# Optimization experiments

Measured on AMD Instinct MI355X. Metric: run time of the kernel, lower is better.

Reference implementation:

```python
import jax, jax.numpy as jnp
from jax import lax
import numpy as np

IN_CH, OUT_CH, K, STRIDE = 4, 256, 16, 8
D_STATE, D_CONV, EXPAND, HEADDIM = 128, 4, 2, 64
D_INNER = EXPAND * OUT_CH            # 512
NHEADS = D_INNER // HEADDIM          # 8
CONV_DIM = D_INNER + 2 * D_STATE     # 768 (ngroups=1)
D_IN_PROJ = 2 * D_INNER + 2 * D_STATE + NHEADS  # 1288
B_SZ, L = 8, 16384


def _conv1d(x, w, b, stride, padding):
    y = lax.conv_general_dilated(x, w, (stride,), padding,
                                 dimension_numbers=('NCH', 'OIH', 'NCH'))
    return y + b[None, :, None]


def _mamba2(u, in_proj_w, conv1d_w, conv1d_b, dt_bias, A_log, D_skip, norm_w, out_proj_w):
    # u: (b, l, d_model). Faithful Mamba2 forward (ngroups=1, rmsnorm gated, no biases on projections).
    b, l, _ = u.shape
    zxbcdt = jnp.einsum('bld,ed->ble', u, in_proj_w)           # (b, l, d_in_proj)
    z = zxbcdt[..., :D_INNER]
    xBC = zxbcdt[..., D_INNER:D_INNER + CONV_DIM]
    dt = jax.nn.softplus(zxbcdt[..., D_INNER + CONV_DIM:] + dt_bias)  # (b, l, h)
    # causal depthwise conv (torch pads d_conv-1 both sides then truncates to :l == left-pad only) + SiLU
    xBC = lax.conv_general_dilated(xBC.transpose(0, 2, 1), conv1d_w, (1,),
                                   [(D_CONV - 1, 0)], feature_group_count=CONV_DIM,
                                   dimension_numbers=('NCH', 'OIH', 'NCH'))
    xBC = jax.nn.silu((xBC + conv1d_b[None, :, None]).transpose(0, 2, 1))  # (b, l, conv_dim)
    xs = xBC[..., :D_INNER].reshape(b, l, NHEADS, HEADDIM)
    Bm = xBC[..., D_INNER:D_INNER + D_STATE]                   # (b, l, n)
    Cm = xBC[..., D_INNER + D_STATE:]                          # (b, l, n)
    A = -jnp.exp(A_log)                                        # (h,), scalar A per head
    dA = jnp.exp(dt * A)                                       # (b, l, h)

    def step(h, inp):
        dA_t, dt_t, x_t, B_t, C_t = inp
        h = h * dA_t[:, :, None, None] + jnp.einsum('bh,bhp,bn->bhpn', dt_t, x_t, B_t)
        return h, jnp.einsum('bhpn,bn->bhp', h, C_t)

    h0 = jnp.zeros((b, NHEADS, HEADDIM, D_STATE), dtype=u.dtype)
    _, ys = lax.scan(step, h0, (dA.swapaxes(0, 1), dt.swapaxes(0, 1),
                                xs.swapaxes(0, 1), Bm.swapaxes(0, 1), Cm.swapaxes(0, 1)))
    y = ys.swapaxes(0, 1) + D_skip[None, None, :, None] * xs   # (b, l, h, p)
    y = y.reshape(b, l, D_INNER) * jax.nn.silu(z)              # gated RMSNorm (norm_before_gate=False)
    y = y * lax.rsqrt(jnp.mean(y * y, axis=-1, keepdims=True) + 1e-5) * norm_w
    return jnp.einsum('ble,de->bld', y, out_proj_w)


def _forward(x, conv_w, conv_b, in_proj_w, conv1d_w, conv1d_b, dt_bias, A_log,
             D_skip, norm_w, out_proj_w, conv1_w, conv1_b, convT_w, convT_b):
    h = jax.nn.relu(_conv1d(x, conv_w, conv_b, STRIDE, 'VALID'))       # (b, out_ch, l')
    y = _mamba2(h.transpose(0, 2, 1), in_proj_w, conv1d_w, conv1d_b,
                dt_bias, A_log, D_skip, norm_w, out_proj_w)
    y = y.transpose(0, 2, 1)                                           # (b, out_ch, l')
    y = _conv1d(y, conv1_w, conv1_b, 1, [(7, 8)])  # torch padding='same', even kernel: left=7, right=8
    # ConvTranspose1d: torch weight (Cin, Cout, K) -> flipped OIH kernel + lhs dilation
    kern = jnp.flip(convT_w, -1).transpose(1, 0, 2)
    y = lax.conv_general_dilated(y, kern, (1,), [(K - 1, K - 1)], lhs_dilation=(STRIDE,),
                                 dimension_numbers=('NCH', 'OIH', 'NCH'))
    return y + convT_b[None, :, None]


def setup_inputs() -> dict:
    key = jax.random.key(0)
    ks = jax.random.split(key, 16)
    n = lambda k, shp, sc=0.05: jax.random.normal(k, shp, dtype=jnp.float32) * sc
    return {
        'x': jax.random.normal(ks[0], (B_SZ, IN_CH, L), dtype=jnp.float32),
        'conv_w': n(ks[1], (OUT_CH, IN_CH, K)),
        'conv_b': n(ks[2], (OUT_CH,)),
        'in_proj_w': n(ks[3], (D_IN_PROJ, OUT_CH)),
        'conv1d_w': n(ks[4], (CONV_DIM, 1, D_CONV), 0.3),
        'conv1d_b': n(ks[5], (CONV_DIM,), 0.1),
        'dt_bias': n(ks[6], (NHEADS,), 0.5),
        'A_log': jnp.log(jax.random.uniform(ks[7], (NHEADS,), minval=1.0, maxval=16.0)),
        'D_skip': n(ks[8], (NHEADS,), 1.0),
        'norm_w': jnp.ones((D_INNER,), dtype=jnp.float32),
        'out_proj_w': n(ks[9], (OUT_CH, D_INNER)),
        'conv1_w': n(ks[10], (STRIDE, OUT_CH, K)),
        'conv1_b': n(ks[11], (STRIDE,)),
        'convT_w': n(ks[12], (STRIDE, IN_CH, K)),
        'convT_b': n(ks[13], (IN_CH,)),
    }


def reference(x, conv_w, conv_b, in_proj_w, conv1d_w, conv1d_b, dt_bias, A_log,
              D_skip, norm_w, out_proj_w, conv1_w, conv1_b, convT_w, convT_b):
    return _forward(x, conv_w, conv_b, in_proj_w, conv1d_w, conv1d_b, dt_bias, A_log,
                    D_skip, norm_w, out_proj_w, conv1_w, conv1_b, convT_w, convT_b)
```

## Files before the change

### kernel.cpp

```cpp
#include <hip/hip_runtime.h>
#include <cstddef>
#include <cstdint>

constexpr int L_IN   = 16384;
constexpr int L_SEQ  = 2047;
constexpr int BATCH  = 8;
constexpr int M_TOK  = BATCH * L_SEQ;
constexpr int D_INNER = 512;
constexpr int NHEADS  = 8;
constexpr int HEADDIM = 64;
constexpr int D_STATE = 128;
constexpr int CONV_DIM = 768;
constexpr int D_IN_PROJ = 1288;

constexpr int QC  = 64;
constexpr int NCH = 32;

constexpr size_t OFF_U    = 0;
constexpr size_t OFF_PB   = OFF_U   + 2096128;
constexpr size_t OFF_ZB   = OFF_U   + 4192256;
constexpr size_t OFF_XBC  = OFF_ZB  + 4192256;
constexpr size_t OFF_DT   = OFF_XBC + 6288384;
constexpr size_t OFF_AW   = OFF_DT  + 131008;
constexpr size_t OFF_XC   = OFF_AW  + 131008;
constexpr size_t OFF_Y    = OFF_XC  + 6288384;
constexpr size_t OFF_YC1  = OFF_Y   + 4192256;
constexpr size_t OFF_PBUF = OFF_YC1 + 131008;
constexpr size_t OFF_HS   = OFF_PBUF + 2048;
constexpr size_t OFF_WBIN = OFF_HS  + 8388608;
constexpr size_t OFF_WBF  = OFF_WBIN + 164864;
constexpr size_t OFF_W2   = OFF_WBF + 8192;

using short8 = __attribute__((ext_vector_type(8))) short;
using f32x4  = __attribute__((ext_vector_type(4))) float;
typedef unsigned short ushort_t;

__device__ __forceinline__ ushort_t f2bf(float f) {
  uint32_t u = __float_as_uint(f);
  u += 0x7fffu + ((u >> 16) & 1u);
  return (ushort_t)(u >> 16);
}
__device__ __forceinline__ float bf2f(ushort_t h) {
  return __uint_as_float(((uint32_t)h) << 16);
}
#define MFMA16(a, b, c) __builtin_amdgcn_mfma_f32_16x16x32_bf16(a, b, c, 0, 0, 0)

#define GLD_LDS(gp, lp) __builtin_amdgcn_global_load_lds( \
    (const __attribute__((address_space(1))) void*)(gp),  \
    (__attribute__((address_space(3))) void*)(lp), 16, 0, 0)

__global__ __launch_bounds__(256) void k_prep(const float* __restrict__ x,
    const float* __restrict__ w1, const float* __restrict__ w3,
    const float* __restrict__ conv1_w, const float* __restrict__ wout,
    ushort_t* __restrict__ PB, ushort_t* __restrict__ o1, ushort_t* __restrict__ o3,
    ushort_t* __restrict__ W2b) {
  const int bid = blockIdx.x;
  const int tid = threadIdx.x;
  if (bid < 512) {
    int idx = bid * 256 + tid;
    if (idx >= M_TOK * 8) return;
    int oct = idx & 7, row = idx >> 3;
    int t = row % L_SEQ, b = row / L_SEQ;
    int ic = oct >> 1, k0 = (oct & 1) * 8;
    const float* src = x + ((size_t)b * 4 + ic) * L_IN + t * 8 + k0;
    float4 a0 = *(const float4*)src;
    float4 a1 = *(const float4*)(src + 4);
    short8 o;
    o[0] = (short)f2bf(a0.x); o[1] = (short)f2bf(a0.y);
    o[2] = (short)f2bf(a0.z); o[3] = (short)f2bf(a0.w);
    o[4] = (short)f2bf(a1.x); o[5] = (short)f2bf(a1.y);
    o[6] = (short)f2bf(a1.z); o[7] = (short)f2bf(a1.w);
    *(short8*)(PB + (size_t)row * 64 + oct * 8) = o;
  } else if (bid < 1800) {
    int i = (bid - 512) * 256 + tid;
    if (i < D_IN_PROJ * 256) o1[i] = f2bf(w1[i]);
    if (i < 256 * 64)        o3[i] = f2bf(w3[i]);
  } else {
    const int r = bid - 1800;
    const int oc = r >> 4, k = r & 15;
    const int d0 = tid;
    float acc0 = 0.f, acc1 = 0.f;
    for (int o = 0; o < 256; o++) {
      float wv = conv1_w[((size_t)oc * 256 + o) * 16 + k];
      acc0 = fmaf(wv, wout[(size_t)o * 512 + d0], acc0);
      acc1 = fmaf(wv, wout[(size_t)o * 512 + d0 + 256], acc1);
    }
    W2b[(size_t)r * 512 + d0]       = f2bf(acc0);
    W2b[(size_t)r * 512 + d0 + 256] = f2bf(acc1);
  }
}

template<int EPI>
__global__ __launch_bounds__(256) void gemm_bf16(const ushort_t* __restrict__ A, int lda,
    const ushort_t* __restrict__ B, int ldb, float* __restrict__ C,
    const float* __restrict__ bias, int M, int N, int K, int nx,
    ushort_t* __restrict__ zb, ushort_t* __restrict__ xbcb,
    float* __restrict__ dtb, float* __restrict__ awb,
    const float* __restrict__ dt_bias, const float* __restrict__ A_log) {
  __shared__ __attribute__((aligned(16))) ushort_t sA[128 * 64];
  __shared__ __attribute__((aligned(16))) ushort_t sB[128 * 64];
  const int tid = threadIdx.x;
  const int cpx = gridDim.x >> 3;
  const int swz = (blockIdx.x & 7) * cpx + (blockIdx.x >> 3);
  const int m0 = (swz / nx) * 128, n0 = (swz % nx) * 128;
  const int w = tid >> 6, lane = tid & 63;
  const int l15 = lane & 15, lK = lane >> 4;
  const int wr = w >> 1, wc = w & 1;
  f32x4 acc[4][4] = {};
  for (int k0 = 0; k0 < K; k0 += 64) {
    __syncthreads();
#pragma unroll
    for (int j = 0; j < 4; j++) {
      int idx = j * 256 + tid;
      int r = idx >> 3;
      int ss = (idx & 7) ^ (r & 7);
      GLD_LDS(A + (size_t)(m0 + r) * lda + k0 + ss * 8, &sA[(j * 256 + w * 64) * 8]);
      GLD_LDS(B + (size_t)(n0 + r) * ldb + k0 + ss * 8, &sB[(j * 256 + w * 64) * 8]);
    }
    __syncthreads();
#pragma unroll
    for (int kk = 0; kk < 2; kk++) {
      short8 af[4], bf[4];
#pragma unroll
      for (int mt = 0; mt < 4; mt++) {
        int r = wr * 64 + mt * 16 + l15;
        af[mt] = *(const short8*)&sA[r * 64 + (((kk * 4 + lK) ^ (r & 7)) * 8)];
      }
#pragma unroll
      for (int nt = 0; nt < 4; nt++) {
        int r = wc * 64 + nt * 16 + l15;
        bf[nt] = *(const short8*)&sB[r * 64 + (((kk * 4 + lK) ^ (r & 7)) * 8)];
      }
#pragma unroll
      for (int mt = 0; mt < 4; mt++)
#pragma unroll
        for (int nt = 0; nt < 4; nt++)
          acc[mt][nt] = MFMA16(af[mt], bf[nt], acc[mt][nt]);
    }
  }
  if constexpr (EPI == 0) {
#pragma unroll
    for (int mt = 0; mt < 4; mt++)
#pragma unroll
      for (int i = 0; i < 4; i++) {
        int gm = m0 + wr * 64 + mt * 16 + lK * 4 + i;
        if (gm < M) {
          float* crow = C + (size_t)gm * N;
#pragma unroll
          for (int nt = 0; nt < 4; nt++) {
            int gn = n0 + wc * 64 + nt * 16 + l15;
            if (gn < N) crow[gn] = acc[mt][nt][i];
          }
        }
      }
  } else if constexpr (EPI == 1) {
    ushort_t* Cb = (ushort_t*)C;
#pragma unroll
    for (int mt = 0; mt < 4; mt++)
#pragma unroll
      for (int i = 0; i < 4; i++) {
        int gm = m0 + wr * 64 + mt * 16 + lK * 4 + i;
#pragma unroll
        for (int nt = 0; nt < 4; nt++) {
          int gn = n0 + wc * 64 + nt * 16 + l15;
          float v = fmaxf(acc[mt][nt][i] + bias[gn], 0.f);
          uint32_t mine = f2bf(v);
          uint32_t other = (uint32_t)__shfl_xor((int)mine, 1, 64);
          if (((lane & 1) == 0) && gm < M)
            *(uint32_t*)(Cb + (size_t)gm * N + gn) = mine | (other << 16);
        }
      }
  } else {
    if (n0 < 1280) {
      ushort_t* dst = (n0 < 512) ? zb : xbcb;
      const int ldd  = (n0 < 512) ? 512 : 768;
      const int coff = (n0 < 512) ? 0 : 512;
#pragma unroll
      for (int mt = 0; mt < 4; mt++)
#pragma unroll
        for (int i = 0; i < 4; i++) {
          int gm = m0 + wr * 64 + mt * 16 + lK * 4 + i;
#pragma unroll
          for (int nt = 0; nt < 4; nt++) {
            int gn = n0 + wc * 64 + nt * 16 + l15;
            uint32_t mine = f2bf(acc[mt][nt][i]);
            uint32_t other = (uint32_t)__shfl_xor((int)mine, 1, 64);
            if (((lane & 1) == 0) && gm < M)
              *(uint32_t*)(dst + (size_t)gm * ldd + (gn - coff)) = mine | (other << 16);
          }
        }
    } else {
#pragma unroll
      for (int mt = 0; mt < 4; mt++)
#pragma unroll
        for (int i = 0; i < 4; i++) {
          int gm = m0 + wr * 64 + mt * 16 + lK * 4 + i;
          if (gm >= M) continue;
#pragma unroll
          for (int nt = 0; nt < 4; nt++) {
            int gn = n0 + wc * 64 + nt * 16 + l15;
            if (gn < N) {
              int hd = gn - 1280;
              float v = acc[mt][nt][i] + dt_bias[hd];
              float sp = (v > 20.f) ? v : log1pf(expf(v));
              dtb[(size_t)gm * 8 + hd] = sp;
              awb[(size_t)gm * 8 + hd] = -expf(A_log[hd]) * sp;
            }
          }
        }
    }
  }
}

__global__ __launch_bounds__(192) void k_dw(const ushort_t* __restrict__ xbcb,
    const float* __restrict__ w, const float* __restrict__ bias,
    ushort_t* __restrict__ xcb) {
  const int bid = blockIdx.x;
  const int tb = bid & 511, b = bid >> 9;
  const int t0 = tb * 4;
  const int c = threadIdx.x * 4;
  const size_t rowb = (size_t)b * L_SEQ;
  float wr[4][4];
#pragma unroll
  for (int j = 0; j < 4; j++)
#pragma unroll
    for (int k = 0; k < 4; k++) wr[j][k] = w[(c + j) * 4 + k];
  const float4 bs = {bias[c], bias[c + 1], bias[c + 2], bias[c + 3]};
  float v[7][4];
#pragma unroll
  for (int r = 0; r < 7; r++) {
    int tt = t0 - 3 + r;
    if (tt >= 0 && tt < L_SEQ) {
      uint2 pk = *(const uint2*)(xbcb + (rowb + tt) * CONV_DIM + c);
      v[r][0] = bf2f((ushort_t)(pk.x & 0xffff));
      v[r][1] = bf2f((ushort_t)(pk.x >> 16));
      v[r][2] = bf2f((ushort_t)(pk.y & 0xffff));
      v[r][3] = bf2f((ushort_t)(pk.y >> 16));
    } else {
      v[r][0] = v[r][1] = v[r][2] = v[r][3] = 0.f;
    }
  }
#pragma unroll
  for (int o = 0; o < 4; o++) {
    int t = t0 + o;
    if (t >= L_SEQ) break;
    float a0 = bs.x, a1 = bs.y, a2 = bs.z, a3 = bs.w;
#pragma unroll
    for (int k = 0; k < 4; k++) {
      a0 = fmaf(v[o + k][0], wr[0][k], a0);
      a1 = fmaf(v[o + k][1], wr[1][k], a1);
      a2 = fmaf(v[o + k][2], wr[2][k], a2);
      a3 = fmaf(v[o + k][3], wr[3][k], a3);
    }
    float s0 = a0 / (1.f + expf(-a0));
    float s1 = a1 / (1.f + expf(-a1));
    float s2 = a2 / (1.f + expf(-a2));
    float s3 = a3 / (1.f + expf(-a3));
    uint2 ov;
    ov.x = (uint32_t)f2bf(s0) | ((uint32_t)f2bf(s1) << 16);
    ov.y = (uint32_t)f2bf(s2) | ((uint32_t)f2bf(s3) << 16);
    *(uint2*)(xcb + (rowb + t) * CONV_DIM + c) = ov;
  }
}

__global__ __launch_bounds__(256) void k_ssd_state(const ushort_t* __restrict__ xcb,
    const float* __restrict__ dtb, const float* __restrict__ aw,
    ushort_t* __restrict__ HSb, float* __restrict__ Pbuf) {
  const int ch = blockIdx.x, bh = blockIdx.y;
  const int b = bh >> 3, h = bh & 7;
  const int t0 = ch * QC;
  const int valid = (L_SEQ - t0 < QC) ? (L_SEQ - t0) : QC;
  const size_t rowbase = (size_t)b * L_SEQ;
  __shared__ __attribute__((aligned(16))) short sBT[128][72];
  __shared__ __attribute__((aligned(16))) short sXw[64][72];
  __shared__ float sW[64];
  __shared__ float sLtot;
  const int tid = threadIdx.x;
  if (tid < 64) {
    float aa = 0.f, dd = 0.f;
    if (tid < valid) { size_t r8 = (rowbase + t0 + tid) * 8 + h; aa = aw[r8]; dd = dtb[r8]; }
    float s = aa;
#pragma unroll
    for (int d = 1; d < 64; d <<= 1) { float o = __shfl_up(s, d, 64); if (tid >= d) s += o; }
    float Lt = __shfl(s, 63, 64);
    sW[tid] = expf(Lt - s) * dd;
    if (tid == 63) sLtot = s;
  }
  __syncthreads();
  for (int i = tid; i < 64 * 16; i += 256) {
    int r = i >> 4, q = (i & 15) * 8;
    short8 v = {0, 0, 0, 0, 0, 0, 0, 0};
    if (r < valid) v = *(const short8*)(xcb + (rowbase + t0 + r) * CONV_DIM + 512 + q);
#pragma unroll
    for (int j = 0; j < 8; j++) sBT[q + j][r] = v[j];
  }
  for (int i = tid; i < 64 * 8; i += 256) {
    int r = i >> 3, q = (i & 7) * 8;
    short8 v = {0, 0, 0, 0, 0, 0, 0, 0};
    if (r < valid) v = *(const short8*)(xcb + (rowbase + t0 + r) * CONV_DIM + h * 64 + q);
    float wv = sW[r];
#pragma unroll
    for (int j = 0; j < 8; j++) sXw[q + j][r] = (short)f2bf(bf2f((ushort_t)v[j]) * wv);
  }
  __syncthreads();
  const int w = tid >> 6, l15 = tid & 15, lK = (tid & 63) >> 4;
  f32x4 acc[2][4] = {};
  short8 afr[2][2];
#pragma unroll
  for (int j = 0; j < 2; j++)
#pragma unroll
    for (int kt = 0; kt < 2; kt++)
      afr[j][kt] = *(const short8*)&sBT[(w * 2 + j) * 16 + l15][kt * 32 + lK * 8];
#pragma unroll
  for (int pt = 0; pt < 4; pt++) {
#pragma unroll
    for (int kt = 0; kt < 2; kt++) {
      short8 bfr = *(const short8*)&sXw[pt * 16 + l15][kt * 32 + lK * 8];
      acc[0][pt] = MFMA16(afr[0][kt], bfr, acc[0][pt]);
      acc[1][pt] = MFMA16(afr[1][kt], bfr, acc[1][pt]);
    }
  }
  ushort_t* dst = HSb + ((size_t)bh * NCH + ch) * 8192;
#pragma unroll
  for (int j = 0; j < 2; j++)
#pragma unroll
    for (int pt = 0; pt < 4; pt++)
#pragma unroll
      for (int i = 0; i < 4; i++) {
        int n = (w * 2 + j) * 16 + lK * 4 + i, p = pt * 16 + l15;
        uint32_t mine = f2bf(acc[j][pt][i]);
        uint32_t other = (uint32_t)__shfl_xor((int)mine, 1, 64);
        if ((l15 & 1) == 0)
          *(uint32_t*)(dst + n * 64 + p) = mine | (other << 16);
      }
  if (tid == 0) Pbuf[bh * NCH + ch] = expf(sLtot);
}

__global__ __launch_bounds__(256) void k_ssd_comb(ushort_t* __restrict__ HSb,
                                                  const float* __restrict__ Pbuf) {
  const int bh = blockIdx.y;
  const int e2 = blockIdx.x * 256 + threadIdx.x;
  const size_t base = (size_t)bh * NCH * 8192 + (size_t)e2 * 2;
  uint32_t pk[NCH];
  float P[NCH];
#pragma unroll
  for (int c = 0; c < NCH; c++) pk[c] = *(const uint32_t*)(HSb + base + (size_t)c * 8192);
#pragma unroll
  for (int c = 0; c < NCH; c++) P[c] = Pbuf[bh * NCH + c];
  float run0 = 0.f, run1 = 0.f;
#pragma unroll
  for (int c = 0; c < NCH; c++) {
    run0 = fmaf(P[c], run0, bf2f((ushort_t)(pk[c] & 0xffff)));
    run1 = fmaf(P[c], run1, bf2f((ushort_t)(pk[c] >> 16)));
    pk[c] = (uint32_t)f2bf(run0) | ((uint32_t)f2bf(run1) << 16);
  }
#pragma unroll
  for (int c = 0; c < NCH; c++) *(uint32_t*)(HSb + base + (size_t)c * 8192) = pk[c];
}

__global__ __launch_bounds__(256) void k_ssd_y(const ushort_t* __restrict__ xcb,
    const float* __restrict__ dtb, const float* __restrict__ aw,
    const float* __restrict__ Dskip, const ushort_t* __restrict__ HSb,
    ushort_t* __restrict__ y16) {
  const int ch = blockIdx.x, bh = blockIdx.y;
  const int b = bh >> 3, h = bh & 7;
  const int t0 = ch * QC;
  const int valid = (L_SEQ - t0 < QC) ? (L_SEQ - t0) : QC;
  const size_t rowbase = (size_t)b * L_SEQ;
  __shared__ __attribute__((aligned(16))) short sB[64][136];
  __shared__ __attribute__((aligned(16))) short sC[64][136];
  __shared__ __attribute__((aligned(16))) short sH[64][136];
  __shared__ __attribute__((aligned(16))) short sX[64][72];
  __shared__ float sLrel[64], sdt[64], sEL[64];
  short (*sM)[72] = (short(*)[72])&sB[0][0];
  const int tid = threadIdx.x;
  if (tid < 64) {
    float aa = 0.f, dd = 0.f;
    if (tid < valid) { size_t r8 = (rowbase + t0 + tid) * 8 + h; aa = aw[r8]; dd = dtb[r8]; }
    float s = aa;
#pragma unroll
    for (int d = 1; d < 64; d <<= 1) { float o = __shfl_up(s, d, 64); if (tid >= d) s += o; }
    sLrel[tid] = s; sdt[tid] = dd; sEL[tid] = expf(s);
  }
  for (int i = tid; i < 64 * 16; i += 256) {
    int r = i >> 4, q = (i & 15) * 8;
    short8 vb = {0, 0, 0, 0, 0, 0, 0, 0}, vc = {0, 0, 0, 0, 0, 0, 0, 0};
    if (r < valid) {
      const ushort_t* rp = xcb + (rowbase + t0 + r) * CONV_DIM;
      vb = *(const short8*)(rp + 512 + q);
      vc = *(const short8*)(rp + 640 + q);
    }
#pragma unroll
    for (int j = 0; j < 8; j++) { sB[r][q + j] = vb[j]; sC[r][q + j] = vc[j]; }
  }
  for (int i = tid; i < 64 * 8; i += 256) {
    int r = i >> 3, q = (i & 7) * 8;
    short8 v = {0, 0, 0, 0, 0, 0, 0, 0};
    if (r < valid) v = *(const short8*)(xcb + (rowbase + t0 + r) * CONV_DIM + h * 64 + q);
#pragma unroll
    for (int j = 0; j < 8; j++) sX[q + j][r] = v[j];
  }
  for (int i = tid; i < 128 * 8; i += 256) {
    int n = i >> 3, q = (i & 7) * 8;
    short8 v = {0, 0, 0, 0, 0, 0, 0, 0};
    if (ch > 0) v = *(const short8*)(HSb + ((size_t)bh * NCH + (ch - 1)) * 8192 + n * 64 + q);
#pragma unroll
    for (int j = 0; j < 8; j++) sH[q + j][n] = v[j];
  }
  __syncthreads();
  const int w = tid >> 6, l15 = tid & 15, lK = (tid & 63) >> 4;
  short8 aC[4];
#pragma unroll
  for (int kt = 0; kt < 4; kt++)
    aC[kt] = *(const short8*)&sC[w * 16 + l15][kt * 32 + lK * 8];
  f32x4 g[4] = {};
#pragma unroll
  for (int st = 0; st < 4; st++)
#pragma unroll
    for (int kt = 0; kt < 4; kt++)
      g[st] = MFMA16(aC[kt], *(const short8*)&sB[st * 16 + l15][kt * 32 + lK * 8], g[st]);
  __syncthreads();
#pragma unroll
  for (int st = 0; st < 4; st++)
#pragma unroll
    for (int i = 0; i < 4; i++) {
      int tt = w * 16 + lK * 4 + i, ss = st * 16 + l15;
      float f = (ss <= tt) ? expf(sLrel[tt] - sLrel[ss]) * sdt[ss] : 0.f;
      sM[tt][ss] = (short)f2bf(g[st][i] * f);
    }
  __syncthreads();
  f32x4 acc[4] = {};
#pragma unroll
  for (int pt = 0; pt < 4; pt++)
#pragma unroll
    for (int kt = 0; kt < 4; kt++)
      acc[pt] = MFMA16(aC[kt], *(const short8*)&sH[pt * 16 + l15][kt * 32 + lK * 8], acc[pt]);
#pragma unroll
  for (int pt = 0; pt < 4; pt++)
#pragma unroll
    for (int i = 0; i < 4; i++)
      acc[pt][i] *= sEL[w * 16 + lK * 4 + i];
  short8 aM[2];
#pragma unroll
  for (int kt = 0; kt < 2; kt++)
    aM[kt] = *(const short8*)&sM[w * 16 + l15][kt * 32 + lK * 8];
#pragma unroll
  for (int pt = 0; pt < 4; pt++)
#pragma unroll
    for (int kt = 0; kt < 2; kt++)
      acc[pt] = MFMA16(aM[kt], *(const short8*)&sX[pt * 16 + l15][kt * 32 + lK * 8], acc[pt]);
  const float Dsk = Dskip[h];
#pragma unroll
  for (int pt = 0; pt < 4; pt++)
#pragma unroll
    for (int i = 0; i < 4; i++) {
      int tt = w * 16 + lK * 4 + i;
      int pp = pt * 16 + l15;
      float v = acc[pt][i] + Dsk * bf2f((ushort_t)sX[pp][tt]);
      uint32_t mine = f2bf(v);
      uint32_t other = (uint32_t)__shfl_xor((int)mine, 1, 64);
      if (((l15 & 1) == 0) && tt < valid)
        *(uint32_t*)(y16 + (rowbase + t0 + tt) * D_INNER + h * 64 + pp) = mine | (other << 16);
    }
}

__global__ __launch_bounds__(256) void k_norm(ushort_t* __restrict__ y16,
    const ushort_t* __restrict__ zb, const float* __restrict__ norm_w) {
  const int row = blockIdx.x * 4 + (threadIdx.x >> 6);
  const int lane = threadIdx.x & 63;
  const int c0 = lane * 8;
  ushort_t* yrow = y16 + (size_t)row * D_INNER;
  short8 yv = *(const short8*)(yrow + c0);
  short8 zv = *(const short8*)(zb + (size_t)row * 512 + c0);
  float v[8];
  float ss = 0.f;
#pragma unroll
  for (int j = 0; j < 8; j++) {
    float z = bf2f((ushort_t)zv[j]);
    float g = z / (1.f + expf(-z));
    v[j] = bf2f((ushort_t)yv[j]) * g;
    ss += v[j] * v[j];
  }
#pragma unroll
  for (int m = 32; m >= 1; m >>= 1) ss += __shfl_xor(ss, m, 64);
  float scale = rsqrtf(ss * (1.f / 512.f) + 1e-5f);
  float4 nw0 = *(const float4*)(norm_w + c0);
  float4 nw1 = *(const float4*)(norm_w + c0 + 4);
  short8 o;
  o[0] = (short)f2bf(v[0] * scale * nw0.x); o[1] = (short)f2bf(v[1] * scale * nw0.y);
  o[2] = (short)f2bf(v[2] * scale * nw0.z); o[3] = (short)f2bf(v[3] * scale * nw0.w);
  o[4] = (short)f2bf(v[4] * scale * nw1.x); o[5] = (short)f2bf(v[5] * scale * nw1.y);
  o[6] = (short)f2bf(v[6] * scale * nw1.z); o[7] = (short)f2bf(v[7] * scale * nw1.w);
  *(short8*)(yrow + c0) = o;
}

__global__ void k_red(const float* __restrict__ Y, const float* __restrict__ b1,
                      float* __restrict__ yc1) {
  int idx = blockIdx.x * 256 + threadIdx.x;
  if (idx >= BATCH * 8 * L_SEQ) return;
  int t = idx % L_SEQ;
  int bj = idx / L_SEQ;
  int j = bj & 7, b = bj >> 3;
  float acc = b1[j];
  const float* Yb = Y + (size_t)b * L_SEQ * 128;
#pragma unroll
  for (int k = 0; k < 16; k++) {
    int tt = t - 7 + k;
    if (tt >= 0 && tt < L_SEQ) acc += Yb[(size_t)tt * 128 + j * 16 + k];
  }
  yc1[idx] = acc;
}

__global__ void k_convT(const float* __restrict__ yc1,
                        const float* __restrict__ wT,
                        const float* __restrict__ bT, float* __restrict__ out) {
  const int s = blockIdx.x * 256 + threadIdx.x;
  const int c = blockIdx.y, b = blockIdx.z;
  float acc = bT[c];
  const int k0 = (15 - (s & 7)) & 7;
#pragma unroll
  for (int dk = 0; dk < 2; dk++) {
    int k = k0 + 8 * dk;
    int num = s - 15 + k;
    int m = num >> 3;
    if (num >= 0 && m < L_SEQ) {
#pragma unroll
      for (int j = 0; j < 8; j++) {
        float v = yc1[((size_t)b * 8 + j) * L_SEQ + m];
        acc = fmaf(v, wT[((size_t)j * 4 + c) * 16 + (15 - k)], acc);
      }
    }
  }
  out[((size_t)b * 4 + c) * L_IN + s] = acc;
}

extern "C" void kernel_launch(void* const* d_in, const int* in_sizes, int n_in,
                              void* d_out, int out_size, void* d_ws, size_t ws_size,
                              hipStream_t stream) {
  const float* x         = (const float*)d_in[0];
  const float* conv_w    = (const float*)d_in[1];
  const float* conv_b    = (const float*)d_in[2];
  const float* in_proj_w = (const float*)d_in[3];
  const float* conv1d_w  = (const float*)d_in[4];
  const float* conv1d_b  = (const float*)d_in[5];
  const float* dt_bias   = (const float*)d_in[6];
  const float* A_log     = (const float*)d_in[7];
  const float* D_skip    = (const float*)d_in[8];
  const float* norm_w    = (const float*)d_in[9];
  const float* out_proj_w= (const float*)d_in[10];
  const float* conv1_w   = (const float*)d_in[11];
  const float* conv1_b   = (const float*)d_in[12];
  const float* convT_w   = (const float*)d_in[13];
  const float* convT_b   = (const float*)d_in[14];
  float* out = (float*)d_out;
  float* ws  = (float*)d_ws;

  ushort_t* ub   = (ushort_t*)(ws + OFF_U);
  ushort_t* PB   = (ushort_t*)(ws + OFF_PB);
  ushort_t* zb   = (ushort_t*)(ws + OFF_ZB);
  ushort_t* xbcb = (ushort_t*)(ws + OFF_XBC);
  float* dtb  = ws + OFF_DT;
  float* awb  = ws + OFF_AW;
  ushort_t* xcb = (ushort_t*)(ws + OFF_XC);
  ushort_t* y16 = (ushort_t*)(ws + OFF_Y);
  float* yc1  = ws + OFF_YC1;
  float* Pbuf = ws + OFF_PBUF;
  ushort_t* HSb = (ushort_t*)(ws + OFF_HS);
  ushort_t* wbin  = (ushort_t*)(ws + OFF_WBIN);
  ushort_t* wbf   = (ushort_t*)(ws + OFF_WBF);
  ushort_t* W2b   = (ushort_t*)(ws + OFF_W2);
  float* Yg   = ws + OFF_U;

  k_prep<<<dim3(1928), 256, 0, stream>>>(x, in_proj_w, conv_w, conv1_w, out_proj_w,
                                         PB, wbin, wbf, W2b);
  gemm_bf16<1><<<dim3(256), 256, 0, stream>>>(PB, 64, wbf, 64, (float*)ub,
      conv_b, M_TOK, 256, 64, 2, nullptr, nullptr, nullptr, nullptr, nullptr, nullptr);
  gemm_bf16<2><<<dim3(1408), 256, 0, stream>>>(ub, 256, wbin, 256, nullptr,
      nullptr, M_TOK, D_IN_PROJ, 256, 11, zb, xbcb, dtb, awb, dt_bias, A_log);
  k_dw<<<dim3(BATCH * 512), 192, 0, stream>>>(xbcb, conv1d_w, conv1d_b, xcb);
  k_ssd_state<<<dim3(NCH, 64), 256, 0, stream>>>(xcb, dtb, awb, HSb, Pbuf);
  k_ssd_comb<<<dim3(16, 64), 256, 0, stream>>>(HSb, Pbuf);
  k_ssd_y<<<dim3(NCH, 64), 256, 0, stream>>>(xcb, dtb, awb, D_skip, HSb, y16);
  k_norm<<<dim3(M_TOK / 4), 256, 0, stream>>>(y16, zb, norm_w);
  gemm_bf16<0><<<dim3(128), 256, 0, stream>>>(y16, 512, W2b, 512, Yg,
      nullptr, M_TOK, 128, D_INNER, 1, nullptr, nullptr, nullptr, nullptr, nullptr, nullptr);
  k_red<<<dim3((BATCH * 8 * L_SEQ + 255) / 256), 256, 0, stream>>>(Yg, conv1_b, yc1);
  k_convT<<<dim3(64, 4, 8), 256, 0, stream>>>(yc1, convT_w, convT_b, out);
}
```

Baseline: 199.2 us.

## Fuse depthwise conv into SSD kernels, norm into out GEMM, tail reduction into convT

```diff
diff --git a/kernel.cpp b/kernel.cpp
--- a/kernel.cpp
+++ b/kernel.cpp
@@ -43,6 +43,7 @@
 __device__ __forceinline__ float bf2f(ushort_t h) {
   return __uint_as_float(((uint32_t)h) << 16);
 }
+__device__ __forceinline__ float siluf(float a) { return a / (1.f + expf(-a)); }
 #define MFMA16(a, b, c) __builtin_amdgcn_mfma_f32_16x16x32_bf16(a, b, c, 0, 0, 0)
 
 #define GLD_LDS(gp, lp) __builtin_amdgcn_global_load_lds( \
@@ -52,6 +53,7 @@
 __global__ __launch_bounds__(256) void k_prep(const float* __restrict__ x,
     const float* __restrict__ w1, const float* __restrict__ w3,
     const float* __restrict__ conv1_w, const float* __restrict__ wout,
+    const float* __restrict__ norm_w,
     ushort_t* __restrict__ PB, ushort_t* __restrict__ o1, ushort_t* __restrict__ o3,
     ushort_t* __restrict__ W2b) {
   const int bid = blockIdx.x;
@@ -85,8 +87,8 @@
       acc0 = fmaf(wv, wout[(size_t)o * 512 + d0], acc0);
       acc1 = fmaf(wv, wout[(size_t)o * 512 + d0 + 256], acc1);
     }
-    W2b[(size_t)r * 512 + d0]       = f2bf(acc0);
-    W2b[(size_t)r * 512 + d0 + 256] = f2bf(acc1);
+    W2b[(size_t)r * 512 + d0]       = f2bf(acc0 * norm_w[d0]);
+    W2b[(size_t)r * 512 + d0 + 256] = f2bf(acc1 * norm_w[d0 + 256]);
   }
 }
 
@@ -138,22 +140,7 @@
           acc[mt][nt] = MFMA16(af[mt], bf[nt], acc[mt][nt]);
     }
   }
-  if constexpr (EPI == 0) {
-#pragma unroll
-    for (int mt = 0; mt < 4; mt++)
-#pragma unroll
-      for (int i = 0; i < 4; i++) {
-        int gm = m0 + wr * 64 + mt * 16 + lK * 4 + i;
-        if (gm < M) {
-          float* crow = C + (size_t)gm * N;
-#pragma unroll
-          for (int nt = 0; nt < 4; nt++) {
-            int gn = n0 + wc * 64 + nt * 16 + l15;
-            if (gn < N) crow[gn] = acc[mt][nt][i];
-          }
-        }
-      }
-  } else if constexpr (EPI == 1) {
+  if constexpr (EPI == 1) {
     ushort_t* Cb = (ushort_t*)C;
 #pragma unroll
     for (int mt = 0; mt < 4; mt++)
@@ -212,58 +199,8 @@
   }
 }
 
-__global__ __launch_bounds__(192) void k_dw(const ushort_t* __restrict__ xbcb,
-    const float* __restrict__ w, const float* __restrict__ bias,
-    ushort_t* __restrict__ xcb) {
-  const int bid = blockIdx.x;
-  const int tb = bid & 511, b = bid >> 9;
-  const int t0 = tb * 4;
-  const int c = threadIdx.x * 4;
-  const size_t rowb = (size_t)b * L_SEQ;
-  float wr[4][4];
-#pragma unroll
-  for (int j = 0; j < 4; j++)
-#pragma unroll
-    for (int k = 0; k < 4; k++) wr[j][k] = w[(c + j) * 4 + k];
-  const float4 bs = {bias[c], bias[c + 1], bias[c + 2], bias[c + 3]};
-  float v[7][4];
-#pragma unroll
-  for (int r = 0; r < 7; r++) {
-    int tt = t0 - 3 + r;
-    if (tt >= 0 && tt < L_SEQ) {
-      uint2 pk = *(const uint2*)(xbcb + (rowb + tt) * CONV_DIM + c);
-      v[r][0] = bf2f((ushort_t)(pk.x & 0xffff));
-      v[r][1] = bf2f((ushort_t)(pk.x >> 16));
-      v[r][2] = bf2f((ushort_t)(pk.y & 0xffff));
-      v[r][3] = bf2f((ushort_t)(pk.y >> 16));
-    } else {
-      v[r][0] = v[r][1] = v[r][2] = v[r][3] = 0.f;
-    }
-  }
-#pragma unroll
-  for (int o = 0; o < 4; o++) {
-    int t = t0 + o;
-    if (t >= L_SEQ) break;
-    float a0 = bs.x, a1 = bs.y, a2 = bs.z, a3 = bs.w;
-#pragma unroll
-    for (int k = 0; k < 4; k++) {
-      a0 = fmaf(v[o + k][0], wr[0][k], a0);
-      a1 = fmaf(v[o + k][1], wr[1][k], a1);
-      a2 = fmaf(v[o + k][2], wr[2][k], a2);
-      a3 = fmaf(v[o + k][3], wr[3][k], a3);
-    }
-    float s0 = a0 / (1.f + expf(-a0));
-    float s1 = a1 / (1.f + expf(-a1));
-    float s2 = a2 / (1.f + expf(-a2));
-    float s3 = a3 / (1.f + expf(-a3));
-    uint2 ov;
-    ov.x = (uint32_t)f2bf(s0) | ((uint32_t)f2bf(s1) << 16);
-    ov.y = (uint32_t)f2bf(s2) | ((uint32_t)f2bf(s3) << 16);
-    *(uint2*)(xcb + (rowb + t) * CONV_DIM + c) = ov;
-  }
-}
-
-__global__ __launch_bounds__(256) void k_ssd_state(const ushort_t* __restrict__ xcb,
+__global__ __launch_bounds__(256) void k_ssd_state(const ushort_t* __restrict__ xbcb,
+    const float* __restrict__ cw, const float* __restrict__ cb,
     const float* __restrict__ dtb, const float* __restrict__ aw,
     ushort_t* __restrict__ HSb, float* __restrict__ Pbuf) {
   const int ch = blockIdx.x, bh = blockIdx.y;
@@ -275,6 +212,8 @@
   __shared__ __attribute__((aligned(16))) short sXw[64][72];
   __shared__ float sW[64];
   __shared__ float sLtot;
+  __shared__ __attribute__((aligned(16))) float sWw[192][4];
+  __shared__ float sWb[192];
   const int tid = threadIdx.x;
   if (tid < 64) {
     float aa = 0.f, dd = 0.f;
@@ -286,21 +225,56 @@
     sW[tid] = expf(Lt - s) * dd;
     if (tid == 63) sLtot = s;
   }
+  for (int i = tid; i < 192; i += 256) {
+    int gc = (i < 128) ? 512 + i : h * 64 + (i - 128);
+    *(float4*)&sWw[i][0] = *(const float4*)(cw + (size_t)gc * 4);
+    sWb[i] = cb[gc];
+  }
   __syncthreads();
   for (int i = tid; i < 64 * 16; i += 256) {
     int r = i >> 4, q = (i & 15) * 8;
-    short8 v = {0, 0, 0, 0, 0, 0, 0, 0};
-    if (r < valid) v = *(const short8*)(xcb + (rowbase + t0 + r) * CONV_DIM + 512 + q);
-#pragma unroll
-    for (int j = 0; j < 8; j++) sBT[q + j][r] = v[j];
+    if (r < valid) {
+      float a[8];
+#pragma unroll
+      for (int j = 0; j < 8; j++) a[j] = sWb[q + j];
+#pragma unroll
+      for (int k = 0; k < 4; k++) {
+        int tt = t0 + r - 3 + k;
+        if (tt >= 0) {
+          short8 v = *(const short8*)(xbcb + (rowbase + tt) * CONV_DIM + 512 + q);
+#pragma unroll
+          for (int j = 0; j < 8; j++) a[j] = fmaf(bf2f((ushort_t)v[j]), sWw[q + j][k], a[j]);
+        }
+      }
+#pragma unroll
+      for (int j = 0; j < 8; j++) sBT[q + j][r] = (short)f2bf(siluf(a[j]));
+    } else {
+#pragma unroll
+      for (int j = 0; j < 8; j++) sBT[q + j][r] = 0;
+    }
   }
   for (int i = tid; i < 64 * 8; i += 256) {
     int r = i >> 3, q = (i & 7) * 8;
-    short8 v = {0, 0, 0, 0, 0, 0, 0, 0};
-    if (r < valid) v = *(const short8*)(xcb + (rowbase + t0 + r) * CONV_DIM + h * 64 + q);
-    float wv = sW[r];
-#pragma unroll
-    for (int j = 0; j < 8; j++) sXw[q + j][r] = (short)f2bf(bf2f((ushort_t)v[j]) * wv);
+    if (r < valid) {
+      float a[8];
+#pragma unroll
+      for (int j = 0; j < 8; j++) a[j] = sWb[128 + q + j];
+#pragma unroll
+      for (int k = 0; k < 4; k++) {
+        int tt = t0 + r - 3 + k;
+        if (tt >= 0) {
+          short8 v = *(const short8*)(xbcb + (rowbase + tt) * CONV_DIM + h * 64 + q);
+#pragma unroll
+          for (int j = 0; j < 8; j++) a[j] = fmaf(bf2f((ushort_t)v[j]), sWw[128 + q + j][k], a[j]);
+        }
+      }
+      float wv = sW[r];
+#pragma unroll
+      for (int j = 0; j < 8; j++) sXw[q + j][r] = (short)f2bf(siluf(a[j]) * wv);
+    } else {
+#pragma unroll
+      for (int j = 0; j < 8; j++) sXw[q + j][r] = 0;
+    }
   }
   __syncthreads();
   const int w = tid >> 6, l15 = tid & 15, lK = (tid & 63) >> 4;
@@ -358,7 +332,8 @@
   for (int c = 0; c < NCH; c++) *(uint32_t*)(HSb + base + (size_t)c * 8192) = pk[c];
 }
 
-__global__ __launch_bounds__(256) void k_ssd_y(const ushort_t* __restrict__ xcb,
+__global__ __launch_bounds__(256) void k_ssd_y(const ushort_t* __restrict__ xbcb,
+    const float* __restrict__ cw, const float* __restrict__ cb,
     const float* __restrict__ dtb, const float* __restrict__ aw,
     const float* __restrict__ Dskip, const ushort_t* __restrict__ HSb,
     ushort_t* __restrict__ y16) {
@@ -372,6 +347,8 @@
   __shared__ __attribute__((aligned(16))) short sH[64][136];
   __shared__ __attribute__((aligned(16))) short sX[64][72];
   __shared__ float sLrel[64], sdt[64], sEL[64];
+  __shared__ __attribute__((aligned(16))) float sWw[320][4];
+  __shared__ float sWb[320];
   short (*sM)[72] = (short(*)[72])&sB[0][0];
   const int tid = threadIdx.x;
   if (tid < 64) {
@@ -382,23 +359,63 @@
     for (int d = 1; d < 64; d <<= 1) { float o = __shfl_up(s, d, 64); if (tid >= d) s += o; }
     sLrel[tid] = s; sdt[tid] = dd; sEL[tid] = expf(s);
   }
+  for (int i = tid; i < 320; i += 256) {
+    int gc = (i < 256) ? 512 + i : h * 64 + (i - 256);
+    *(float4*)&sWw[i][0] = *(const float4*)(cw + (size_t)gc * 4);
+    sWb[i] = cb[gc];
+  }
+  __syncthreads();
   for (int i = tid; i < 64 * 16; i += 256) {
     int r = i >> 4, q = (i & 15) * 8;
-    short8 vb = {0, 0, 0, 0, 0, 0, 0, 0}, vc = {0, 0, 0, 0, 0, 0, 0, 0};
     if (r < valid) {
-      const ushort_t* rp = xcb + (rowbase + t0 + r) * CONV_DIM;
-      vb = *(const short8*)(rp + 512 + q);
-      vc = *(const short8*)(rp + 640 + q);
-    }
-#pragma unroll
-    for (int j = 0; j < 8; j++) { sB[r][q + j] = vb[j]; sC[r][q + j] = vc[j]; }
+      float ab[8], ac[8];
+#pragma unroll
+      for (int j = 0; j < 8; j++) { ab[j] = sWb[q + j]; ac[j] = sWb[128 + q + j]; }
+#pragma unroll
+      for (int k = 0; k < 4; k++) {
+        int tt = t0 + r - 3 + k;
+        if (tt >= 0) {
+          const ushort_t* rp = xbcb + (rowbase + tt) * CONV_DIM;
+          short8 vb = *(const short8*)(rp + 512 + q);
+          short8 vc = *(const short8*)(rp + 640 + q);
+#pragma unroll
+          for (int j = 0; j < 8; j++) {
+            ab[j] = fmaf(bf2f((ushort_t)vb[j]), sWw[q + j][k], ab[j]);
+            ac[j] = fmaf(bf2f((ushort_t)vc[j]), sWw[128 + q + j][k], ac[j]);
+          }
+        }
+      }
+#pragma unroll
+      for (int j = 0; j < 8; j++) {
+        sB[r][q + j] = (short)f2bf(siluf(ab[j]));
+        sC[r][q + j] = (short)f2bf(siluf(ac[j]));
+      }
+    } else {
+#pragma unroll
+      for (int j = 0; j < 8; j++) { sB[r][q + j] = 0; sC[r][q + j] = 0; }
+    }
   }
   for (int i = tid; i < 64 * 8; i += 256) {
     int r = i >> 3, q = (i & 7) * 8;
-    short8 v = {0, 0, 0, 0, 0, 0, 0, 0};
-    if (r < valid) v = *(const short8*)(xcb + (rowbase + t0 + r) * CONV_DIM + h * 64 + q);
-#pragma unroll
-    for (int j = 0; j < 8; j++) sX[q + j][r] = v[j];
+    if (r < valid) {
+      float a[8];
+#pragma unroll
+      for (int j = 0; j < 8; j++) a[j] = sWb[256 + q + j];
+#pragma unroll
+      for (int k = 0; k < 4; k++) {
+        int tt = t0 + r - 3 + k;
+        if (tt >= 0) {
+          short8 v = *(const short8*)(xbcb + (rowbase + tt) * CONV_DIM + h * 64 + q);
+#pragma unroll
+          for (int j = 0; j < 8; j++) a[j] = fmaf(bf2f((ushort_t)v[j]), sWw[256 + q + j][k], a[j]);
+        }
+      }
+#pragma unroll
+      for (int j = 0; j < 8; j++) sX[q + j][r] = (short)f2bf(siluf(a[j]));
+    } else {
+#pragma unroll
+      for (int j = 0; j < 8; j++) sX[q + j][r] = 0;
+    }
   }
   for (int i = tid; i < 128 * 8; i += 256) {
     int n = i >> 3, q = (i & 7) * 8;
@@ -464,74 +481,146 @@
     }
 }
 
-__global__ __launch_bounds__(256) void k_norm(ushort_t* __restrict__ y16,
-    const ushort_t* __restrict__ zb, const float* __restrict__ norm_w) {
-  const int row = blockIdx.x * 4 + (threadIdx.x >> 6);
-  const int lane = threadIdx.x & 63;
-  const int c0 = lane * 8;
-  ushort_t* yrow = y16 + (size_t)row * D_INNER;
-  short8 yv = *(const short8*)(yrow + c0);
-  short8 zv = *(const short8*)(zb + (size_t)row * 512 + c0);
-  float v[8];
-  float ss = 0.f;
-#pragma unroll
-  for (int j = 0; j < 8; j++) {
-    float z = bf2f((ushort_t)zv[j]);
-    float g = z / (1.f + expf(-z));
-    v[j] = bf2f((ushort_t)yv[j]) * g;
-    ss += v[j] * v[j];
-  }
-#pragma unroll
-  for (int m = 32; m >= 1; m >>= 1) ss += __shfl_xor(ss, m, 64);
-  float scale = rsqrtf(ss * (1.f / 512.f) + 1e-5f);
-  float4 nw0 = *(const float4*)(norm_w + c0);
-  float4 nw1 = *(const float4*)(norm_w + c0 + 4);
-  short8 o;
-  o[0] = (short)f2bf(v[0] * scale * nw0.x); o[1] = (short)f2bf(v[1] * scale * nw0.y);
-  o[2] = (short)f2bf(v[2] * scale * nw0.z); o[3] = (short)f2bf(v[3] * scale * nw0.w);
-  o[4] = (short)f2bf(v[4] * scale * nw1.x); o[5] = (short)f2bf(v[5] * scale * nw1.y);
-  o[6] = (short)f2bf(v[6] * scale * nw1.z); o[7] = (short)f2bf(v[7] * scale * nw1.w);
-  *(short8*)(yrow + c0) = o;
-}
-
-__global__ void k_red(const float* __restrict__ Y, const float* __restrict__ b1,
-                      float* __restrict__ yc1) {
-  int idx = blockIdx.x * 256 + threadIdx.x;
-  if (idx >= BATCH * 8 * L_SEQ) return;
-  int t = idx % L_SEQ;
-  int bj = idx / L_SEQ;
-  int j = bj & 7, b = bj >> 3;
-  float acc = b1[j];
-  const float* Yb = Y + (size_t)b * L_SEQ * 128;
-#pragma unroll
-  for (int k = 0; k < 16; k++) {
-    int tt = t - 7 + k;
-    if (tt >= 0 && tt < L_SEQ) acc += Yb[(size_t)tt * 128 + j * 16 + k];
-  }
-  yc1[idx] = acc;
-}
-
-__global__ void k_convT(const float* __restrict__ yc1,
-                        const float* __restrict__ wT,
-                        const float* __restrict__ bT, float* __restrict__ out) {
-  const int s = blockIdx.x * 256 + threadIdx.x;
-  const int c = blockIdx.y, b = blockIdx.z;
-  float acc = bT[c];
-  const int k0 = (15 - (s & 7)) & 7;
-#pragma unroll
-  for (int dk = 0; dk < 2; dk++) {
-    int k = k0 + 8 * dk;
-    int num = s - 15 + k;
-    int m = num >> 3;
-    if (num >= 0 && m < L_SEQ) {
-#pragma unroll
-      for (int j = 0; j < 8; j++) {
-        float v = yc1[((size_t)b * 8 + j) * L_SEQ + m];
-        acc = fmaf(v, wT[((size_t)j * 4 + c) * 16 + (15 - k)], acc);
-      }
-    }
-  }
-  out[((size_t)b * 4 + c) * L_IN + s] = acc;
+__global__ __launch_bounds__(256) void gemm_out(const ushort_t* __restrict__ y16,
+    const ushort_t* __restrict__ zb, const ushort_t* __restrict__ W2b,
+    float* __restrict__ Yg) {
+  __shared__ __attribute__((aligned(16))) ushort_t sA[128 * 64];
+  __shared__ __attribute__((aligned(16))) ushort_t sB[128 * 64];
+  __shared__ float sSum[128];
+  const int tid = threadIdx.x;
+  const int cpx = gridDim.x >> 3;
+  const int m0 = ((blockIdx.x & 7) * cpx + (blockIdx.x >> 3)) * 128;
+  const int w = tid >> 6, lane = tid & 63;
+  const int l15 = lane & 15, lK = lane >> 4;
+  const int wr = w >> 1, wc = w & 1;
+  f32x4 acc[4][4] = {};
+  float psum[4] = {0.f, 0.f, 0.f, 0.f};
+  for (int k0 = 0; k0 < 512; k0 += 64) {
+    __syncthreads();
+#pragma unroll
+    for (int j = 0; j < 4; j++) {
+      int idx = j * 256 + tid;
+      int r = idx >> 3, s = idx & 7;
+      int ssb = s ^ (r & 7);
+      GLD_LDS(W2b + (size_t)r * 512 + k0 + ssb * 8, &sB[(j * 256 + w * 64) * 8]);
+      size_t goff = (size_t)(m0 + r) * 512 + k0 + s * 8;
+      short8 yv = *(const short8*)(y16 + goff);
+      short8 zv = *(const short8*)(zb + goff);
+      short8 o;
+#pragma unroll
+      for (int t = 0; t < 8; t++) {
+        float vv = bf2f((ushort_t)yv[t]) * siluf(bf2f((ushort_t)zv[t]));
+        psum[j] = fmaf(vv, vv, psum[j]);
+        o[t] = (short)f2bf(vv);
+      }
+      *(short8*)&sA[r * 64 + ((s ^ (r & 7)) * 8)] = o;
+    }
+    __syncthreads();
+#pragma unroll
+    for (int kk = 0; kk < 2; kk++) {
+      short8 af[4], bf[4];
+#pragma unroll
+      for (int mt = 0; mt < 4; mt++) {
+        int r = wr * 64 + mt * 16 + l15;
+        af[mt] = *(const short8*)&sA[r * 64 + (((kk * 4 + lK) ^ (r & 7)) * 8)];
+      }
+#pragma unroll
+      for (int nt = 0; nt < 4; nt++) {
+        int r = wc * 64 + nt * 16 + l15;
+        bf[nt] = *(const short8*)&sB[r * 64 + (((kk * 4 + lK) ^ (r & 7)) * 8)];
+      }
+#pragma unroll
+      for (int mt = 0; mt < 4; mt++)
+#pragma unroll
+        for (int nt = 0; nt < 4; nt++)
+          acc[mt][nt] = MFMA16(af[mt], bf[nt], acc[mt][nt]);
+    }
+  }
+#pragma unroll
+  for (int j = 0; j < 4; j++) {
+    float s = psum[j];
+    s += __shfl_xor(s, 1, 64);
+    s += __shfl_xor(s, 2, 64);
+    s += __shfl_xor(s, 4, 64);
+    if ((tid & 7) == 0) sSum[j * 32 + (tid >> 3)] = s;
+  }
+  __syncthreads();
+#pragma unroll
+  for (int mt = 0; mt < 4; mt++)
+#pragma unroll
+    for (int i = 0; i < 4; i++) {
+      int rl = wr * 64 + mt * 16 + lK * 4 + i;
+      int gm = m0 + rl;
+      if (gm < M_TOK) {
+        float scale = rsqrtf(sSum[rl] * (1.f / 512.f) + 1e-5f);
+        float* crow = Yg + (size_t)gm * 128;
+#pragma unroll
+        for (int nt = 0; nt < 4; nt++) {
+          int gn = wc * 64 + nt * 16 + l15;
+          crow[gn] = acc[mt][nt][i] * scale;
+        }
+      }
+    }
+}
+
+__global__ __launch_bounds__(256) void k_tail(const float* __restrict__ Yg,
+    const float* __restrict__ b1, const float* __restrict__ wT,
+    const float* __restrict__ bT, float* __restrict__ out) {
+  const int bid = blockIdx.x;
+  const int sc = bid & 31, b = bid >> 5;
+  const int s0 = sc * 512;
+  const int mbase = (s0 - 15) >> 3;
+  const int tid = threadIdx.x;
+  __shared__ float sY[8][66];
+  __shared__ float swT[8][4][16];
+  __shared__ float sb1[8], sbT[4];
+  for (int i = tid; i < 512; i += 256) {
+    int j = i >> 6, c = (i >> 4) & 3, k = i & 15;
+    swT[j][c][k] = wT[((size_t)j * 4 + c) * 16 + k];
+  }
+  if (tid < 8) sb1[tid] = b1[tid];
+  if (tid < 4) sbT[tid] = bT[tid];
+  __syncthreads();
+  const float* Yb = Yg + (size_t)b * L_SEQ * 128;
+  for (int item = tid; item < 8 * 66; item += 256) {
+    int j = item / 66, ii = item % 66;
+    int m = mbase + ii;
+    float acc = 0.f;
+    if ((unsigned)m < (unsigned)L_SEQ) {
+      acc = sb1[j];
+#pragma unroll
+      for (int k = 0; k < 16; k++) {
+        int tt = m - 7 + k;
+        if ((unsigned)tt < (unsigned)L_SEQ) acc += Yb[(size_t)tt * 128 + j * 16 + k];
+      }
+    }
+    sY[j][ii] = acc;
+  }
+  __syncthreads();
+  const int c = tid >> 6, si = tid & 63;
+  float ov[8];
+#pragma unroll
+  for (int u = 0; u < 8; u++) {
+    int s = s0 + si * 8 + u;
+    float acc = sbT[c];
+    const int k0 = (15 - u) & 7;
+#pragma unroll
+    for (int dk = 0; dk < 2; dk++) {
+      int k = k0 + 8 * dk;
+      int num = s - 15 + k;
+      int m = num >> 3;
+      if (num >= 0 && m < L_SEQ) {
+        int ii = m - mbase;
+#pragma unroll
+        for (int j = 0; j < 8; j++)
+          acc = fmaf(sY[j][ii], swT[j][c][15 - k], acc);
+      }
+    }
+    ov[u] = acc;
+  }
+  float* op = out + ((size_t)b * 4 + c) * L_IN + s0 + si * 8;
+  *(float4*)op       = *(float4*)&ov[0];
+  *(float4*)(op + 4) = *(float4*)&ov[4];
 }
 
 extern "C" void kernel_launch(void* const* d_in, const int* in_sizes, int n_in,
@@ -561,9 +650,7 @@
   ushort_t* xbcb = (ushort_t*)(ws + OFF_XBC);
   float* dtb  = ws + OFF_DT;
   float* awb  = ws + OFF_AW;
-  ushort_t* xcb = (ushort_t*)(ws + OFF_XC);
   ushort_t* y16 = (ushort_t*)(ws + OFF_Y);
-  float* yc1  = ws + OFF_YC1;
   float* Pbuf = ws + OFF_PBUF;
   ushort_t* HSb = (ushort_t*)(ws + OFF_HS);
   ushort_t* wbin  = (ushort_t*)(ws + OFF_WBIN);
@@ -572,18 +659,16 @@
   float* Yg   = ws + OFF_U;
 
   k_prep<<<dim3(1928), 256, 0, stream>>>(x, in_proj_w, conv_w, conv1_w, out_proj_w,
-                                         PB, wbin, wbf, W2b);
+                                         norm_w, PB, wbin, wbf, W2b);
   gemm_bf16<1><<<dim3(256), 256, 0, stream>>>(PB, 64, wbf, 64, (float*)ub,
       conv_b, M_TOK, 256, 64, 2, nullptr, nullptr, nullptr, nullptr, nullptr, nullptr);
   gemm_bf16<2><<<dim3(1408), 256, 0, stream>>>(ub, 256, wbin, 256, nullptr,
       nullptr, M_TOK, D_IN_PROJ, 256, 11, zb, xbcb, dtb, awb, dt_bias, A_log);
-  k_dw<<<dim3(BATCH * 512), 192, 0, stream>>>(xbcb, conv1d_w, conv1d_b, xcb);
-  k_ssd_state<<<dim3(NCH, 64), 256, 0, stream>>>(xcb, dtb, awb, HSb, Pbuf);
+  k_ssd_state<<<dim3(NCH, 64), 256, 0, stream>>>(xbcb, conv1d_w, conv1d_b,
+                                                 dtb, awb, HSb, Pbuf);
   k_ssd_comb<<<dim3(16, 64), 256, 0, stream>>>(HSb, Pbuf);
-  k_ssd_y<<<dim3(NCH, 64), 256, 0, stream>>>(xcb, dtb, awb, D_skip, HSb, y16);
-  k_norm<<<dim3(M_TOK / 4), 256, 0, stream>>>(y16, zb, norm_w);
-  gemm_bf16<0><<<dim3(128), 256, 0, stream>>>(y16, 512, W2b, 512, Yg,
-      nullptr, M_TOK, 128, D_INNER, 1, nullptr, nullptr, nullptr, nullptr, nullptr, nullptr);
-  k_red<<<dim3((BATCH * 8 * L_SEQ + 255) / 256), 256, 0, stream>>>(Yg, conv1_b, yc1);
-  k_convT<<<dim3(64, 4, 8), 256, 0, stream>>>(yc1, convT_w, convT_b, out);
-}
+  k_ssd_y<<<dim3(NCH, 64), 256, 0, stream>>>(xbcb, conv1d_w, conv1d_b,
+                                             dtb, awb, D_skip, HSb, y16);
+  gemm_out<<<dim3(128), 256, 0, stream>>>(y16, zb, W2b, Yg);
+  k_tail<<<dim3(256), 256, 0, stream>>>(Yg, conv1_b, convT_w, convT_b, out);
+}
```

After: 392.7 us. 1.97x slower.

## Double-buffer GEMM LDS tiles and fuse reduction with transposed conv tail

Applied to the files above, without the earlier changes.

```diff
diff --git a/kernel.cpp b/kernel.cpp
--- a/kernel.cpp
+++ b/kernel.cpp
@@ -43,6 +43,7 @@
 __device__ __forceinline__ float bf2f(ushort_t h) {
   return __uint_as_float(((uint32_t)h) << 16);
 }
+__device__ __forceinline__ float siluf(float a) { return a / (1.f + expf(-a)); }
 #define MFMA16(a, b, c) __builtin_amdgcn_mfma_f32_16x16x32_bf16(a, b, c, 0, 0, 0)
 
 #define GLD_LDS(gp, lp) __builtin_amdgcn_global_load_lds( \
@@ -97,8 +98,8 @@
     ushort_t* __restrict__ zb, ushort_t* __restrict__ xbcb,
     float* __restrict__ dtb, float* __restrict__ awb,
     const float* __restrict__ dt_bias, const float* __restrict__ A_log) {
-  __shared__ __attribute__((aligned(16))) ushort_t sA[128 * 64];
-  __shared__ __attribute__((aligned(16))) ushort_t sB[128 * 64];
+  __shared__ __attribute__((aligned(16))) ushort_t sA[2][128 * 64];
+  __shared__ __attribute__((aligned(16))) ushort_t sB[2][128 * 64];
   const int tid = threadIdx.x;
   const int cpx = gridDim.x >> 3;
   const int swz = (blockIdx.x & 7) * cpx + (blockIdx.x >> 3);
@@ -107,29 +108,35 @@
   const int l15 = lane & 15, lK = lane >> 4;
   const int wr = w >> 1, wc = w & 1;
   f32x4 acc[4][4] = {};
-  for (int k0 = 0; k0 < K; k0 += 64) {
-    __syncthreads();
+
+  auto STAGE = [&](int buf, int k0) {
 #pragma unroll
     for (int j = 0; j < 4; j++) {
       int idx = j * 256 + tid;
       int r = idx >> 3;
       int ss = (idx & 7) ^ (r & 7);
-      GLD_LDS(A + (size_t)(m0 + r) * lda + k0 + ss * 8, &sA[(j * 256 + w * 64) * 8]);
-      GLD_LDS(B + (size_t)(n0 + r) * ldb + k0 + ss * 8, &sB[(j * 256 + w * 64) * 8]);
-    }
-    __syncthreads();
+      GLD_LDS(A + (size_t)(m0 + r) * lda + k0 + ss * 8, &sA[buf][(j * 256 + w * 64) * 8]);
+      GLD_LDS(B + (size_t)(n0 + r) * ldb + k0 + ss * 8, &sB[buf][(j * 256 + w * 64) * 8]);
+    }
+  };
+
+  STAGE(0, 0);
+  __syncthreads();
+  int cur = 0;
+  for (int k0 = 0; k0 < K; k0 += 64) {
+    if (k0 + 64 < K) STAGE(cur ^ 1, k0 + 64);
 #pragma unroll
     for (int kk = 0; kk < 2; kk++) {
       short8 af[4], bf[4];
 #pragma unroll
       for (int mt = 0; mt < 4; mt++) {
         int r = wr * 64 + mt * 16 + l15;
-        af[mt] = *(const short8*)&sA[r * 64 + (((kk * 4 + lK) ^ (r & 7)) * 8)];
+        af[mt] = *(const short8*)&sA[cur][r * 64 + (((kk * 4 + lK) ^ (r & 7)) * 8)];
       }
 #pragma unroll
       for (int nt = 0; nt < 4; nt++) {
         int r = wc * 64 + nt * 16 + l15;
-        bf[nt] = *(const short8*)&sB[r * 64 + (((kk * 4 + lK) ^ (r & 7)) * 8)];
+        bf[nt] = *(const short8*)&sB[cur][r * 64 + (((kk * 4 + lK) ^ (r & 7)) * 8)];
       }
 #pragma unroll
       for (int mt = 0; mt < 4; mt++)
@@ -137,6 +144,8 @@
         for (int nt = 0; nt < 4; nt++)
           acc[mt][nt] = MFMA16(af[mt], bf[nt], acc[mt][nt]);
     }
+    __syncthreads();
+    cur ^= 1;
   }
   if constexpr (EPI == 0) {
 #pragma unroll
@@ -252,13 +261,9 @@
       a2 = fmaf(v[o + k][2], wr[2][k], a2);
       a3 = fmaf(v[o + k][3], wr[3][k], a3);
     }
-    float s0 = a0 / (1.f + expf(-a0));
-    float s1 = a1 / (1.f + expf(-a1));
-    float s2 = a2 / (1.f + expf(-a2));
-    float s3 = a3 / (1.f + expf(-a3));
     uint2 ov;
-    ov.x = (uint32_t)f2bf(s0) | ((uint32_t)f2bf(s1) << 16);
-    ov.y = (uint32_t)f2bf(s2) | ((uint32_t)f2bf(s3) << 16);
+    ov.x = (uint32_t)f2bf(siluf(a0)) | ((uint32_t)f2bf(siluf(a1)) << 16);
+    ov.y = (uint32_t)f2bf(siluf(a2)) | ((uint32_t)f2bf(siluf(a3)) << 16);
     *(uint2*)(xcb + (rowb + t) * CONV_DIM + c) = ov;
   }
 }
@@ -494,44 +499,64 @@
   *(short8*)(yrow + c0) = o;
 }
 
-__global__ void k_red(const float* __restrict__ Y, const float* __restrict__ b1,
-                      float* __restrict__ yc1) {
-  int idx = blockIdx.x * 256 + threadIdx.x;
-  if (idx >= BATCH * 8 * L_SEQ) return;
-  int t = idx % L_SEQ;
-  int bj = idx / L_SEQ;
-  int j = bj & 7, b = bj >> 3;
-  float acc = b1[j];
-  const float* Yb = Y + (size_t)b * L_SEQ * 128;
-#pragma unroll
-  for (int k = 0; k < 16; k++) {
-    int tt = t - 7 + k;
-    if (tt >= 0 && tt < L_SEQ) acc += Yb[(size_t)tt * 128 + j * 16 + k];
-  }
-  yc1[idx] = acc;
-}
-
-__global__ void k_convT(const float* __restrict__ yc1,
-                        const float* __restrict__ wT,
-                        const float* __restrict__ bT, float* __restrict__ out) {
-  const int s = blockIdx.x * 256 + threadIdx.x;
-  const int c = blockIdx.y, b = blockIdx.z;
-  float acc = bT[c];
-  const int k0 = (15 - (s & 7)) & 7;
-#pragma unroll
-  for (int dk = 0; dk < 2; dk++) {
-    int k = k0 + 8 * dk;
-    int num = s - 15 + k;
-    int m = num >> 3;
-    if (num >= 0 && m < L_SEQ) {
-#pragma unroll
-      for (int j = 0; j < 8; j++) {
-        float v = yc1[((size_t)b * 8 + j) * L_SEQ + m];
-        acc = fmaf(v, wT[((size_t)j * 4 + c) * 16 + (15 - k)], acc);
+__global__ __launch_bounds__(256) void k_tail(const float* __restrict__ Yg,
+    const float* __restrict__ b1, const float* __restrict__ wT,
+    const float* __restrict__ bT, float* __restrict__ out) {
+  const int bid = blockIdx.x;
+  const int sc = bid & 31, b = bid >> 5;
+  const int s0 = sc * 512;
+  const int mbase = (s0 - 15) >> 3;
+  const int tid = threadIdx.x;
+  __shared__ float sY[8][66];
+  __shared__ float swT[8][4][16];
+  __shared__ float sb1[8], sbT[4];
+  for (int i = tid; i < 512; i += 256) {
+    int j = i >> 6, c = (i >> 4) & 3, k = i & 15;
+    swT[j][c][k] = wT[((size_t)j * 4 + c) * 16 + k];
+  }
+  if (tid < 8) sb1[tid] = b1[tid];
+  if (tid < 4) sbT[tid] = bT[tid];
+  __syncthreads();
+  const float* Yb = Yg + (size_t)b * L_SEQ * 128;
+  for (int item = tid; item < 8 * 66; item += 256) {
+    int j = item / 66, ii = item % 66;
+    int m = mbase + ii;
+    float acc = 0.f;
+    if ((unsigned)m < (unsigned)L_SEQ) {
+      acc = sb1[j];
+#pragma unroll
+      for (int k = 0; k < 16; k++) {
+        int tt = m - 7 + k;
+        if ((unsigned)tt < (unsigned)L_SEQ) acc += Yb[(size_t)tt * 128 + j * 16 + k];
       }
     }
-  }
-  out[((size_t)b * 4 + c) * L_IN + s] = acc;
+    sY[j][ii] = acc;
+  }
+  __syncthreads();
+  const int c = tid >> 6, si = tid & 63;
+  float ov[8];
+#pragma unroll
+  for (int u = 0; u < 8; u++) {
+    int s = s0 + si * 8 + u;
+    float acc = sbT[c];
+    const int k0 = (15 - u) & 7;
+#pragma unroll
+    for (int dk = 0; dk < 2; dk++) {
+      int k = k0 + 8 * dk;
+      int num = s - 15 + k;
+      int m = num >> 3;
+      if (num >= 0 && m < L_SEQ) {
+        int ii = m - mbase;
+#pragma unroll
+        for (int j = 0; j < 8; j++)
+          acc = fmaf(sY[j][ii], swT[j][c][15 - k], acc);
+      }
+    }
+    ov[u] = acc;
+  }
+  float* op = out + ((size_t)b * 4 + c) * L_IN + s0 + si * 8;
+  *(float4*)op       = *(float4*)&ov[0];
+  *(float4*)(op + 4) = *(float4*)&ov[4];
 }
 
 extern "C" void kernel_launch(void* const* d_in, const int* in_sizes, int n_in,
@@ -563,7 +588,6 @@
   float* awb  = ws + OFF_AW;
   ushort_t* xcb = (ushort_t*)(ws + OFF_XC);
   ushort_t* y16 = (ushort_t*)(ws + OFF_Y);
-  float* yc1  = ws + OFF_YC1;
   float* Pbuf = ws + OFF_PBUF;
   ushort_t* HSb = (ushort_t*)(ws + OFF_HS);
   ushort_t* wbin  = (ushort_t*)(ws + OFF_WBIN);
@@ -584,6 +608,5 @@
   k_norm<<<dim3(M_TOK / 4), 256, 0, stream>>>(y16, zb, norm_w);
   gemm_bf16<0><<<dim3(128), 256, 0, stream>>>(y16, 512, W2b, 512, Yg,
       nullptr, M_TOK, 128, D_INNER, 1, nullptr, nullptr, nullptr, nullptr, nullptr, nullptr);
-  k_red<<<dim3((BATCH * 8 * L_SEQ + 255) / 256), 256, 0, stream>>>(Yg, conv1_b, yc1);
-  k_convT<<<dim3(64, 4, 8), 256, 0, stream>>>(yc1, convT_w, convT_b, out);
-}
+  k_tail<<<dim3(256), 256, 0, stream>>>(Yg, conv1_b, convT_w, convT_b, out);
+}
```

Result: no change. 198.7 us (-0.2%).
